# Kernel optimization log

Hardware: AMD Instinct MI355X
Metric: run time of the kernel (lower is better)

Reference implementation:

```python
import jax, jax.numpy as jnp
import numpy as np

# Static DAG: input -> L hidden layers of K nodes (dense between layers) -> output.
B, WIDTH, K, L = 262144, 64, 4, 4


def _linear_init(key, shape, fan_in):
    # matches nn.Linear default: U(-1/sqrt(fan_in), 1/sqrt(fan_in))
    bound = 1.0 / np.sqrt(fan_in)
    return jax.random.uniform(key, shape, jnp.float32, -bound, bound)


def setup_inputs() -> dict:
    key = jax.random.key(0)
    ks = jax.random.split(key, 9)
    x = jax.random.normal(ks[0], (B, WIDTH), jnp.float32)
    # input node -> first hidden layer (K edges)
    W_in = _linear_init(ks[1], (K, WIDTH, WIDTH), WIDTH)
    b_in = _linear_init(ks[2], (K, WIDTH), WIDTH)
    # between hidden layers: (L-1) transitions, K*K edges each; [pred, node, out, in]
    W_mid = _linear_init(ks[3], (L - 1, K, K, WIDTH, WIDTH), WIDTH)
    b_mid = _linear_init(ks[4], (L - 1, K, K, WIDTH), WIDTH)
    # last hidden layer -> output node (K edges)
    W_out = _linear_init(ks[5], (K, WIDTH, WIDTH), WIDTH)
    b_out = _linear_init(ks[6], (K, WIDTH), WIDTH)
    return {"x": x, "W_in": W_in, "b_in": b_in, "W_mid": W_mid,
            "b_mid": b_mid, "W_out": W_out, "b_out": b_out}


def _l2_normalize(t):
    # torch.linalg.norm(t) with no dim: Frobenius norm over the WHOLE tensor
    return t / jnp.linalg.norm(t)


def reference(x, W_in, b_in, W_mid, b_mid, W_out, b_out):
    # input node -> layer 1: each node k gets a single edge Linear, then normalize
    h = jnp.einsum('bw,kvw->kbv', x, W_in) + b_in[:, None, :]  # [K,B,W]
    h = jax.vmap(_l2_normalize)(h)
    # hidden -> hidden transitions: node v sums over its K predecessor edges
    for l in range(L - 1):  # small fixed structural loop over layers
        pre = jnp.einsum('pbw,pkvw->kbv', h, W_mid[l]) + b_mid[l].sum(axis=0)[:, None, :]
        h = jax.vmap(_l2_normalize)(pre)
    # last layer -> output node: sum K edge outputs, normalize
    out = jnp.einsum('pbw,pvw->bv', h, W_out) + b_out.sum(axis=0)
    return _l2_normalize(out)
```

## Files before the change

kernel.cpp:

```cpp
#include <hip/hip_runtime.h>


#define BF 262144.0f
#define SLOT 4608

#define OFF_G   0
#define OFF_S   4096
#define OFF_P2  8192
#define OFF_C2  73728
#define OFF_P4  74752
#define OFF_C4  91136
#define OFF_MO  91392
#define OFF_CO  95488

typedef __attribute__((ext_vector_type(8))) short bf16x8;
typedef __attribute__((ext_vector_type(4))) float f32x4;

__device__ __forceinline__ unsigned short f2bf(float f) {
  unsigned u = __builtin_bit_cast(unsigned, f);
  u += 0x7FFF + ((u >> 16) & 1);
  return (unsigned short)(u >> 16);
}
__device__ __forceinline__ float bf2f(unsigned short h) {
  unsigned u = ((unsigned)h) << 16;
  return __builtin_bit_cast(float, u);
}

__device__ __forceinline__ bf16x8 cvt8(f32x4 a, f32x4 b, float s) {
  bf16x8 t;
#pragma unroll
  for (int j = 0; j < 4; j++) {
    t[j]     = (short)f2bf(a[j] * s);
    t[j + 4] = (short)f2bf(b[j] * s);
  }
  return t;
}

__device__ __forceinline__ void split8(f32x4 a, f32x4 b, float sc,
                                       bf16x8& hi, bf16x8& lo) {
#pragma unroll
  for (int j = 0; j < 4; j++) {
    float v = a[j] * sc;
    unsigned short h = f2bf(v);
    hi[j] = (short)h; lo[j] = (short)f2bf(v - bf2f(h));
    v = b[j] * sc;
    h = f2bf(v);
    hi[j + 4] = (short)h; lo[j + 4] = (short)f2bf(v - bf2f(h));
  }
}

__device__ __forceinline__ float qpart(const unsigned short* th,
                                       const unsigned short* tl,
                                       int it, int col, int quad,
                                       const float Greg[4][4]) {
  f32x4 dq[4];
#pragma unroll
  for (int ut = 0; ut < 4; ut++) dq[ut] = (f32x4){0.f, 0.f, 0.f, 0.f};
#pragma unroll
  for (int ks = 0; ks < 2; ks++) {
    const bf16x8 ah = *(const bf16x8*)&th[(it * 16 + col) * 72 + ks * 32 + quad * 8];
    const bf16x8 al = *(const bf16x8*)&tl[(it * 16 + col) * 72 + ks * 32 + quad * 8];
#pragma unroll
    for (int ut = 0; ut < 4; ut++) {
      const bf16x8 bh = *(const bf16x8*)&th[(ut * 16 + col) * 72 + ks * 32 + quad * 8];
      const bf16x8 bl = *(const bf16x8*)&tl[(ut * 16 + col) * 72 + ks * 32 + quad * 8];
      dq[ut] = __builtin_amdgcn_mfma_f32_16x16x32_bf16(ah, bh, dq[ut], 0, 0, 0);
      dq[ut] = __builtin_amdgcn_mfma_f32_16x16x32_bf16(ah, bl, dq[ut], 0, 0, 0);
      dq[ut] = __builtin_amdgcn_mfma_f32_16x16x32_bf16(al, bh, dq[ut], 0, 0, 0);
    }
  }
  float qp = 0.f;
#pragma unroll
  for (int ut = 0; ut < 4; ut++)
#pragma unroll
    for (int r = 0; r < 4; r++) qp += dq[ut][r] * Greg[ut][r];
  return qp;
}

__device__ __forceinline__ void blkred(float qp, float* red4, float* qvv,
                                       int idx, int tid, int lane, int it) {
#pragma unroll
  for (int off = 32; off; off >>= 1) qp += __shfl_down(qp, off, 64);
  if (lane == 0) red4[it] = qp;
  __syncthreads();
  if (tid == 0) qvv[idx] = 1.0f / sqrtf(red4[0] + red4[1] + red4[2] + red4[3]);
  __syncthreads();
}

__global__ __launch_bounds__(256) void kG(const float* __restrict__ x,
                                          float* __restrict__ Gpart) {
  __shared__ __align__(16) unsigned short xts[4][4][16][8];
  __shared__ float sred[256][4];
  const int tid = threadIdx.x;
  const int lane = tid & 63, mt = tid >> 6;
  const int col = lane & 15, q = lane >> 4;
  const int row0 = tid >> 4;
  const int cf0  = (tid & 15) * 4;

  f32x4 acc[4];
#pragma unroll
  for (int nt = 0; nt < 4; nt++) acc[nt] = (f32x4){0.f, 0.f, 0.f, 0.f};
  float s0 = 0.f, s1 = 0.f, s2 = 0.f, s3 = 0.f;

  const float* bx = x + (long)blockIdx.x * 32768;
  f32x4 r0 = *(const f32x4*)(bx + tid * 4);
  f32x4 r1 = *(const f32x4*)(bx + 1024 + tid * 4);

  for (int c = 0; c < 16; c++) {
    __syncthreads();
    s0 += r0[0] + r1[0]; s1 += r0[1] + r1[1];
    s2 += r0[2] + r1[2]; s3 += r0[3] + r1[3];
#pragma unroll
    for (int j = 0; j < 4; j++) {
      const int cf = cf0 + j;
      xts[cf >> 4][row0 >> 3][cf & 15][row0 & 7]        = f2bf(r0[j]);
      xts[cf >> 4][2 + (row0 >> 3)][cf & 15][row0 & 7]  = f2bf(r1[j]);
    }
    f32x4 r0n = r0, r1n = r1;
    if (c < 15) {
      r0n = *(const f32x4*)(bx + (c + 1) * 2048 + tid * 4);
      r1n = *(const f32x4*)(bx + (c + 1) * 2048 + 1024 + tid * 4);
    }
    __syncthreads();
    const bf16x8 af = *(const bf16x8*)xts[mt][q][col];
#pragma unroll
    for (int nt = 0; nt < 4; nt++) {
      const bf16x8 bfr = *(const bf16x8*)xts[nt][q][col];
      acc[nt] = __builtin_amdgcn_mfma_f32_16x16x32_bf16(af, bfr, acc[nt], 0, 0, 0);
    }
    r0 = r0n; r1 = r1n;
  }

  float* myp = Gpart + (long)blockIdx.x * 4160;
#pragma unroll
  for (int nt = 0; nt < 4; nt++)
#pragma unroll
    for (int r = 0; r < 4; r++)
      myp[(mt * 16 + q * 4 + r) * 64 + nt * 16 + col] = acc[nt][r];

  sred[tid][0] = s0; sred[tid][1] = s1; sred[tid][2] = s2; sred[tid][3] = s3;
  __syncthreads();
  if (tid < 64) {
    float t = 0.f;
#pragma unroll
    for (int k2 = 0; k2 < 16; k2++) t += sred[(tid >> 2) + 16 * k2][tid & 3];
    myp[4096 + tid] = t;
  }
}

__global__ __launch_bounds__(256) void kGred(const float* __restrict__ Gpart,
                                             float* __restrict__ G,
                                             float* __restrict__ s) {
  __shared__ float red[4][64];
  const int tid = threadIdx.x;
  const int e = blockIdx.x * 64 + (tid & 63);
  const int quarter = tid >> 6;
  float acc = 0.f;
#pragma unroll 4
  for (int j = 0; j < 128; j++)
    acc += Gpart[(long)(quarter * 128 + j) * 4160 + e];
  red[quarter][tid & 63] = acc;
  __syncthreads();
  if (tid < 64) {
    const float t = red[0][tid] + red[1][tid] + red[2][tid] + red[3][tid];
    const int ee = blockIdx.x * 64 + tid;
    if (ee < 4096) G[ee] = t;
    else           s[ee - 4096] = t;
  }
}

__global__ __launch_bounds__(256) void kChainA(
    const float* __restrict__ Win, const float* __restrict__ bin,
    const float* __restrict__ Wm0, const float* __restrict__ bm0,
    const float* __restrict__ Wm1, const float* __restrict__ bm1,
    const float* __restrict__ G, const float* __restrict__ s,
    float* __restrict__ Pout, float* __restrict__ cpout) {
  extern __shared__ __align__(16) char smem[];
  unsigned short* Tth = (unsigned short*)smem;
  unsigned short* Ttl = Tth + 4 * SLOT;
  float* cAv  = (float*)(Ttl + 4 * SLOT);
  float* cBv  = cAv + 256;
  float* slv  = cBv + 64;
  float* red4 = slv + 64;
  float* qvv  = red4 + 4;

  const int tid = threadIdx.x;
  const int p2 = blockIdx.x >> 2, k2 = blockIdx.x & 3;
  const int lane = tid & 63, it = tid >> 6;
  const int col = lane & 15, quad = lane >> 4;

  float Greg[4][4];
#pragma unroll
  for (int ut = 0; ut < 4; ut++)
#pragma unroll
    for (int r = 0; r < 4; r++)
      Greg[ut][r] = G[(it * 16 + quad * 4 + r) * 64 + ut * 16 + col];
  if (tid < 64) slv[tid] = s[tid];
  if (tid < 256) cAv[tid] = bin[tid];

  {
    const int tc = tid >> 2, rb = (tid & 3) * 16;
#pragma unroll
    for (int p = 0; p < 4; p++)
#pragma unroll
      for (int j = 0; j < 16; j++) {
        const float tv = Win[p * 4096 + (rb + j) * 64 + tc];
        const unsigned short h = f2bf(tv);
        Tth[p * SLOT + tc * 72 + rb + j] = h;
        Ttl[p * SLOT + tc * 72 + rb + j] = f2bf(tv - bf2f(h));
      }
  }
  __syncthreads();

#pragma unroll
  for (int p = 0; p < 4; p++) {
    float qp = qpart(Tth + p * SLOT, Ttl + p * SLOT, it, col, quad, Greg);
    if (tid < 64) {
      float sd = 0.f;
      for (int w = 0; w < 64; w++)
        sd += slv[w] * (bf2f(Tth[p * SLOT + w * 72 + tid]) +
                        bf2f(Ttl[p * SLOT + w * 72 + tid]));
      const float c = cAv[p * 64 + tid];
      qp += c * (2.f * sd + BF * c);
    }
    blkred(qp, red4, qvv, p, tid, lane, it);
  }

  f32x4 dc[4];
#pragma unroll
  for (int nt = 0; nt < 4; nt++) dc[nt] = (f32x4){0.f, 0.f, 0.f, 0.f};
  float c2acc = 0.f;

  const int arow = it * 16 + col;
  f32x4 wr[4];
  {
    const float* wbase = Wm0 + (long)((0 * 4 + p2) * 64 + arow) * 64;
    wr[0] = *(const f32x4*)(wbase + quad * 8);
    wr[1] = *(const f32x4*)(wbase + quad * 8 + 4);
    wr[2] = *(const f32x4*)(wbase + 32 + quad * 8);
    wr[3] = *(const f32x4*)(wbase + 36 + quad * 8);
  }
#pragma unroll
  for (int p = 0; p < 4; p++) {
    const float inv = qvv[p];
    bf16x8 awh0, awl0, awh1, awl1;
    split8(wr[0], wr[1], inv, awh0, awl0);
    split8(wr[2], wr[3], inv, awh1, awl1);
    if (p < 3) {
      const float* wbase = Wm0 + (long)(((p + 1) * 4 + p2) * 64 + arow) * 64;
      wr[0] = *(const f32x4*)(wbase + quad * 8);
      wr[1] = *(const f32x4*)(wbase + quad * 8 + 4);
      wr[2] = *(const f32x4*)(wbase + 32 + quad * 8);
      wr[3] = *(const f32x4*)(wbase + 36 + quad * 8);
    }
#pragma unroll
    for (int nt = 0; nt < 4; nt++) {
      const bf16x8 bh0 = *(const bf16x8*)&Tth[p * SLOT + (nt * 16 + col) * 72 + quad * 8];
      const bf16x8 bl0 = *(const bf16x8*)&Ttl[p * SLOT + (nt * 16 + col) * 72 + quad * 8];
      dc[nt] = __builtin_amdgcn_mfma_f32_16x16x32_bf16(awh0, bh0, dc[nt], 0, 0, 0);
      dc[nt] = __builtin_amdgcn_mfma_f32_16x16x32_bf16(awh0, bl0, dc[nt], 0, 0, 0);
      dc[nt] = __builtin_amdgcn_mfma_f32_16x16x32_bf16(awl0, bh0, dc[nt], 0, 0, 0);
      const bf16x8 bh1 = *(const bf16x8*)&Tth[p * SLOT + (nt * 16 + col) * 72 + 32 + quad * 8];
      const bf16x8 bl1 = *(const bf16x8*)&Ttl[p * SLOT + (nt * 16 + col) * 72 + 32 + quad * 8];
      dc[nt] = __builtin_amdgcn_mfma_f32_16x16x32_bf16(awh1, bh1, dc[nt], 0, 0, 0);
      dc[nt] = __builtin_amdgcn_mfma_f32_16x16x32_bf16(awh1, bl1, dc[nt], 0, 0, 0);
      dc[nt] = __builtin_amdgcn_mfma_f32_16x16x32_bf16(awl1, bh1, dc[nt], 0, 0, 0);
    }
    if (tid < 64) {
      const float* wrow = Wm0 + (long)((p * 4 + p2) * 64 + tid) * 64;
      float pc = 0.f;
#pragma unroll
      for (int u4 = 0; u4 < 16; u4++) {
        const f32x4 wv = *(const f32x4*)(wrow + u4 * 4);
        pc += wv[0] * cAv[p * 64 + u4 * 4]     + wv[1] * cAv[p * 64 + u4 * 4 + 1] +
              wv[2] * cAv[p * 64 + u4 * 4 + 2] + wv[3] * cAv[p * 64 + u4 * 4 + 3];
      }
      c2acc += inv * pc + bm0[(p * 4 + p2) * 64 + tid];
    }
  }
  __syncthreads();

#pragma unroll
  for (int nt = 0; nt < 4; nt++)
#pragma unroll
    for (int r = 0; r < 4; r++) {
      const float val = dc[nt][r];
      const unsigned short h = f2bf(val);
      const int w_ = nt * 16 + col, v_ = it * 16 + quad * 4 + r;
      Tth[w_ * 72 + v_] = h;
      Ttl[w_ * 72 + v_] = f2bf(val - bf2f(h));
    }
  if (tid < 64) cBv[tid] = c2acc;
  __syncthreads();

  {
    float qp = qpart(Tth, Ttl, it, col, quad, Greg);
    if (tid < 64) {
      float sd = 0.f;
      for (int w = 0; w < 64; w++)
        sd += slv[w] * (bf2f(Tth[w * 72 + tid]) + bf2f(Ttl[w * 72 + tid]));
      const float c = cBv[tid];
      qp += c * (2.f * sd + BF * c);
    }
    blkred(qp, red4, qvv, 4, tid, lane, it);
  }
  const float inv2 = qvv[4];

  {
    f32x4 dcO[4];
#pragma unroll
    for (int nt = 0; nt < 4; nt++) dcO[nt] = (f32x4){0.f, 0.f, 0.f, 0.f};
    const float* wbase = Wm1 + (long)((p2 * 4 + k2) * 64 + arow) * 64;
    const f32x4 w0 = *(const f32x4*)(wbase + quad * 8);
    const f32x4 w1 = *(const f32x4*)(wbase + quad * 8 + 4);
    const f32x4 w2 = *(const f32x4*)(wbase + 32 + quad * 8);
    const f32x4 w3 = *(const f32x4*)(wbase + 36 + quad * 8);
    bf16x8 awh0, awl0, awh1, awl1;
    split8(w0, w1, inv2, awh0, awl0);
    split8(w2, w3, inv2, awh1, awl1);
#pragma unroll
    for (int nt = 0; nt < 4; nt++) {
      const bf16x8 bh0 = *(const bf16x8*)&Tth[(nt * 16 + col) * 72 + quad * 8];
      const bf16x8 bl0 = *(const bf16x8*)&Ttl[(nt * 16 + col) * 72 + quad * 8];
      dcO[nt] = __builtin_amdgcn_mfma_f32_16x16x32_bf16(awh0, bh0, dcO[nt], 0, 0, 0);
      dcO[nt] = __builtin_amdgcn_mfma_f32_16x16x32_bf16(awh0, bl0, dcO[nt], 0, 0, 0);
      dcO[nt] = __builtin_amdgcn_mfma_f32_16x16x32_bf16(awl0, bh0, dcO[nt], 0, 0, 0);
      const bf16x8 bh1 = *(const bf16x8*)&Tth[(nt * 16 + col) * 72 + 32 + quad * 8];
      const bf16x8 bl1 = *(const bf16x8*)&Ttl[(nt * 16 + col) * 72 + 32 + quad * 8];
      dcO[nt] = __builtin_amdgcn_mfma_f32_16x16x32_bf16(awh1, bh1, dcO[nt], 0, 0, 0);
      dcO[nt] = __builtin_amdgcn_mfma_f32_16x16x32_bf16(awh1, bl1, dcO[nt], 0, 0, 0);
      dcO[nt] = __builtin_amdgcn_mfma_f32_16x16x32_bf16(awl1, bh1, dcO[nt], 0, 0, 0);
    }
    float* po = Pout + (long)(p2 * 4 + k2) * 4096;
#pragma unroll
    for (int nt = 0; nt < 4; nt++)
#pragma unroll
      for (int r = 0; r < 4; r++)
        po[(it * 16 + quad * 4 + r) * 64 + nt * 16 + col] = dcO[nt][r];
    if (tid < 64) {
      const float* wrow = Wm1 + (long)((p2 * 4 + k2) * 64 + tid) * 64;
      float pc = 0.f;
#pragma unroll
      for (int u4 = 0; u4 < 16; u4++) {
        const f32x4 wv = *(const f32x4*)(wrow + u4 * 4);
        pc += wv[0] * cBv[u4 * 4]     + wv[1] * cBv[u4 * 4 + 1] +
              wv[2] * cBv[u4 * 4 + 2] + wv[3] * cBv[u4 * 4 + 3];
      }
      cpout[(p2 * 4 + k2) * 64 + tid] = inv2 * pc + bm1[(p2 * 4 + k2) * 64 + tid];
    }
  }
}

__global__ __launch_bounds__(256) void kChainB(
    const float* __restrict__ Pin, const float* __restrict__ cpin,
    const float* __restrict__ Wm2, const float* __restrict__ bm2,
    const float* __restrict__ Wout, const float* __restrict__ bout,
    const float* __restrict__ G, const float* __restrict__ s,
    float* __restrict__ Pout, float* __restrict__ cpout) {
  extern __shared__ __align__(16) char smem[];
  unsigned short* Tth = (unsigned short*)smem;
  unsigned short* Ttl = Tth + 4 * SLOT;
  float* cAv  = (float*)(Ttl + 4 * SLOT);
  float* cBv  = cAv + 256;
  float* slv  = cBv + 64;
  float* red4 = slv + 64;
  float* qvv  = red4 + 4;

  const int tid = threadIdx.x;
  const int kp = blockIdx.x;
  const int lane = tid & 63, it = tid >> 6;
  const int col = lane & 15, quad = lane >> 4;

  float Greg[4][4];
#pragma unroll
  for (int ut = 0; ut < 4; ut++)
#pragma unroll
    for (int r = 0; r < 4; r++)
      Greg[ut][r] = G[(it * 16 + quad * 4 + r) * 64 + ut * 16 + col];
  if (tid < 64) slv[tid] = s[tid];
  if (tid < 256) {
    const int k = tid >> 6, v = tid & 63;
    cAv[tid] = cpin[(0 * 4 + k) * 64 + v] + cpin[(1 * 4 + k) * 64 + v] +
               cpin[(2 * 4 + k) * 64 + v] + cpin[(3 * 4 + k) * 64 + v];
  }

  {
    const int tc = tid >> 2, rb = (tid & 3) * 16;
#pragma unroll
    for (int k = 0; k < 4; k++)
#pragma unroll
      for (int j = 0; j < 16; j++) {
        const int off = (rb + j) * 64 + tc;
        const float tv = Pin[(0 * 4 + k) * 4096 + off] + Pin[(1 * 4 + k) * 4096 + off] +
                         Pin[(2 * 4 + k) * 4096 + off] + Pin[(3 * 4 + k) * 4096 + off];
        const unsigned short h = f2bf(tv);
        Tth[k * SLOT + tc * 72 + rb + j] = h;
        Ttl[k * SLOT + tc * 72 + rb + j] = f2bf(tv - bf2f(h));
      }
  }
  __syncthreads();

#pragma unroll
  for (int k = 0; k < 4; k++) {
    float qp = qpart(Tth + k * SLOT, Ttl + k * SLOT, it, col, quad, Greg);
    if (tid < 64) {
      float sd = 0.f;
      for (int w = 0; w < 64; w++)
        sd += slv[w] * (bf2f(Tth[k * SLOT + w * 72 + tid]) +
                        bf2f(Ttl[k * SLOT + w * 72 + tid]));
      const float c = cAv[k * 64 + tid];
      qp += c * (2.f * sd + BF * c);
    }
    blkred(qp, red4, qvv, k, tid, lane, it);
  }

  f32x4 dc[4];
#pragma unroll
  for (int nt = 0; nt < 4; nt++) dc[nt] = (f32x4){0.f, 0.f, 0.f, 0.f};
  float c4acc = 0.f;

  const int arow = it * 16 + col;
  f32x4 wr[4];
  {
    const float* wbase = Wm2 + (long)((0 * 4 + kp) * 64 + arow) * 64;
    wr[0] = *(const f32x4*)(wbase + quad * 8);
    wr[1] = *(const f32x4*)(wbase + quad * 8 + 4);
    wr[2] = *(const f32x4*)(wbase + 32 + quad * 8);
    wr[3] = *(const f32x4*)(wbase + 36 + quad * 8);
  }
#pragma unroll
  for (int k = 0; k < 4; k++) {
    const float inv = qvv[k];
    bf16x8 awh0, awl0, awh1, awl1;
    split8(wr[0], wr[1], inv, awh0, awl0);
    split8(wr[2], wr[3], inv, awh1, awl1);
    if (k < 3) {
      const float* wbase = Wm2 + (long)(((k + 1) * 4 + kp) * 64 + arow) * 64;
      wr[0] = *(const f32x4*)(wbase + quad * 8);
      wr[1] = *(const f32x4*)(wbase + quad * 8 + 4);
      wr[2] = *(const f32x4*)(wbase + 32 + quad * 8);
      wr[3] = *(const f32x4*)(wbase + 36 + quad * 8);
    }
#pragma unroll
    for (int nt = 0; nt < 4; nt++) {
      const bf16x8 bh0 = *(const bf16x8*)&Tth[k * SLOT + (nt * 16 + col) * 72 + quad * 8];
      const bf16x8 bl0 = *(const bf16x8*)&Ttl[k * SLOT + (nt * 16 + col) * 72 + quad * 8];
      dc[nt] = __builtin_amdgcn_mfma_f32_16x16x32_bf16(awh0, bh0, dc[nt], 0, 0, 0);
      dc[nt] = __builtin_amdgcn_mfma_f32_16x16x32_bf16(awh0, bl0, dc[nt], 0, 0, 0);
      dc[nt] = __builtin_amdgcn_mfma_f32_16x16x32_bf16(awl0, bh0, dc[nt], 0, 0, 0);
      const bf16x8 bh1 = *(const bf16x8*)&Tth[k * SLOT + (nt * 16 + col) * 72 + 32 + quad * 8];
      const bf16x8 bl1 = *(const bf16x8*)&Ttl[k * SLOT + (nt * 16 + col) * 72 + 32 + quad * 8];
      dc[nt] = __builtin_amdgcn_mfma_f32_16x16x32_bf16(awh1, bh1, dc[nt], 0, 0, 0);
      dc[nt] = __builtin_amdgcn_mfma_f32_16x16x32_bf16(awh1, bl1, dc[nt], 0, 0, 0);
      dc[nt] = __builtin_amdgcn_mfma_f32_16x16x32_bf16(awl1, bh1, dc[nt], 0, 0, 0);
    }
    if (tid < 64) {
      const float* wrow = Wm2 + (long)((k * 4 + kp) * 64 + tid) * 64;
      float pc = 0.f;
#pragma unroll
      for (int u4 = 0; u4 < 16; u4++) {
        const f32x4 wv = *(const f32x4*)(wrow + u4 * 4);
        pc += wv[0] * cAv[k * 64 + u4 * 4]     + wv[1] * cAv[k * 64 + u4 * 4 + 1] +
              wv[2] * cAv[k * 64 + u4 * 4 + 2] + wv[3] * cAv[k * 64 + u4 * 4 + 3];
      }
      c4acc += inv * pc + bm2[(k * 4 + kp) * 64 + tid];
    }
  }
  __syncthreads();

#pragma unroll
  for (int nt = 0; nt < 4; nt++)
#pragma unroll
    for (int r = 0; r < 4; r++) {
      const float val = dc[nt][r];
      const unsigned short h = f2bf(val);
      const int w_ = nt * 16 + col, v_ = it * 16 + quad * 4 + r;
      Tth[w_ * 72 + v_] = h;
      Ttl[w_ * 72 + v_] = f2bf(val - bf2f(h));
    }
  if (tid < 64) cBv[tid] = c4acc;
  __syncthreads();

  {
    float qp = qpart(Tth, Ttl, it, col, quad, Greg);
    if (tid < 64) {
      float sd = 0.f;
      for (int w = 0; w < 64; w++)
        sd += slv[w] * (bf2f(Tth[w * 72 + tid]) + bf2f(Ttl[w * 72 + tid]));
      const float c = cBv[tid];
      qp += c * (2.f * sd + BF * c);
    }
    blkred(qp, red4, qvv, 4, tid, lane, it);
  }
  const float inv4 = qvv[4];

  {
    f32x4 dcO[4];
#pragma unroll
    for (int nt = 0; nt < 4; nt++) dcO[nt] = (f32x4){0.f, 0.f, 0.f, 0.f};
    const float* wbase = Wout + (long)(kp * 64 + arow) * 64;
    const f32x4 w0 = *(const f32x4*)(wbase + quad * 8);
    const f32x4 w1 = *(const f32x4*)(wbase + quad * 8 + 4);
    const f32x4 w2 = *(const f32x4*)(wbase + 32 + quad * 8);
    const f32x4 w3 = *(const f32x4*)(wbase + 36 + quad * 8);
    bf16x8 awh0, awl0, awh1, awl1;
    split8(w0, w1, inv4, awh0, awl0);
    split8(w2, w3, inv4, awh1, awl1);
#pragma unroll
    for (int nt = 0; nt < 4; nt++) {
      const bf16x8 bh0 = *(const bf16x8*)&Tth[(nt * 16 + col) * 72 + quad * 8];
      const bf16x8 bl0 = *(const bf16x8*)&Ttl[(nt * 16 + col) * 72 + quad * 8];
      dcO[nt] = __builtin_amdgcn_mfma_f32_16x16x32_bf16(awh0, bh0, dcO[nt], 0, 0, 0);
      dcO[nt] = __builtin_amdgcn_mfma_f32_16x16x32_bf16(awh0, bl0, dcO[nt], 0, 0, 0);
      dcO[nt] = __builtin_amdgcn_mfma_f32_16x16x32_bf16(awl0, bh0, dcO[nt], 0, 0, 0);
      const bf16x8 bh1 = *(const bf16x8*)&Tth[(nt * 16 + col) * 72 + 32 + quad * 8];
      const bf16x8 bl1 = *(const bf16x8*)&Ttl[(nt * 16 + col) * 72 + 32 + quad * 8];
      dcO[nt] = __builtin_amdgcn_mfma_f32_16x16x32_bf16(awh1, bh1, dcO[nt], 0, 0, 0);
      dcO[nt] = __builtin_amdgcn_mfma_f32_16x16x32_bf16(awh1, bl1, dcO[nt], 0, 0, 0);
      dcO[nt] = __builtin_amdgcn_mfma_f32_16x16x32_bf16(awl1, bh1, dcO[nt], 0, 0, 0);
    }
    float* po = Pout + (long)kp * 4096;
#pragma unroll
    for (int nt = 0; nt < 4; nt++)
#pragma unroll
      for (int r = 0; r < 4; r++)
        po[(it * 16 + quad * 4 + r) * 64 + nt * 16 + col] = dcO[nt][r];
    if (tid < 64) {
      const float* wrow = Wout + (long)(kp * 64 + tid) * 64;
      float pc = 0.f;
#pragma unroll
      for (int u4 = 0; u4 < 16; u4++) {
        const f32x4 wv = *(const f32x4*)(wrow + u4 * 4);
        pc += wv[0] * cBv[u4 * 4]     + wv[1] * cBv[u4 * 4 + 1] +
              wv[2] * cBv[u4 * 4 + 2] + wv[3] * cBv[u4 * 4 + 3];
      }
      cpout[kp * 64 + tid] = inv4 * pc + bout[kp * 64 + tid];
    }
  }
}

__global__ __launch_bounds__(256) void kNorm(const float* __restrict__ Psrc,
                                             const float* __restrict__ csrc,
                                             const float* __restrict__ G,
                                             const float* __restrict__ s,
                                             float* __restrict__ MoS,
                                             float* __restrict__ coS) {
  __shared__ float Tf[64][68];
  __shared__ __align__(16) unsigned short Tth[64][68], Ttl[64][68];
  __shared__ float red[256];
  __shared__ __align__(16) float cl[64], sl[64];
  const int tid = threadIdx.x;
  const int lane = tid & 63, it = tid >> 6;
  const int col = lane & 15, quad = lane >> 4;

  float Greg[4][4];
#pragma unroll
  for (int ut = 0; ut < 4; ut++)
#pragma unroll
    for (int r = 0; r < 4; r++)
      Greg[ut][r] = G[(it * 16 + quad * 4 + r) * 64 + ut * 16 + col];

#pragma unroll
  for (int m = 0; m < 16; m++) {
    const int li = m * 256 + tid;
    Tf[li >> 6][li & 63] = Psrc[li] + Psrc[4096 + li] + Psrc[8192 + li] + Psrc[12288 + li];
  }
  if (tid < 64) {
    cl[tid] = csrc[tid] + csrc[64 + tid] + csrc[128 + tid] + csrc[192 + tid];
    sl[tid] = s[tid];
  }
  __syncthreads();

  {
    const int tc = tid >> 2;
    const int rb = (tid & 3) * 16;
#pragma unroll
    for (int j = 0; j < 16; j++) {
      const float tv = Tf[rb + j][tc];
      const unsigned short h = f2bf(tv);
      Tth[tc][rb + j] = h;
      Ttl[tc][rb + j] = f2bf(tv - bf2f(h));
    }
  }
  __syncthreads();

  float qp = 0.f;
  {
    f32x4 dq[4];
#pragma unroll
    for (int ut = 0; ut < 4; ut++) dq[ut] = (f32x4){0.f, 0.f, 0.f, 0.f};
#pragma unroll
    for (int ks = 0; ks < 2; ks++) {
      const bf16x8 ah = *(const bf16x8*)&Tth[it * 16 + col][ks * 32 + quad * 8];
      const bf16x8 al = *(const bf16x8*)&Ttl[it * 16 + col][ks * 32 + quad * 8];
#pragma unroll
      for (int ut = 0; ut < 4; ut++) {
        const bf16x8 bh = *(const bf16x8*)&Tth[ut * 16 + col][ks * 32 + quad * 8];
        const bf16x8 bl = *(const bf16x8*)&Ttl[ut * 16 + col][ks * 32 + quad * 8];
        dq[ut] = __builtin_amdgcn_mfma_f32_16x16x32_bf16(ah, bh, dq[ut], 0, 0, 0);
        dq[ut] = __builtin_amdgcn_mfma_f32_16x16x32_bf16(ah, bl, dq[ut], 0, 0, 0);
        dq[ut] = __builtin_amdgcn_mfma_f32_16x16x32_bf16(al, bh, dq[ut], 0, 0, 0);
      }
    }
#pragma unroll
    for (int ut = 0; ut < 4; ut++)
#pragma unroll
      for (int r = 0; r < 4; r++)
        qp += dq[ut][r] * Greg[ut][r];
  }
  if (tid < 64) {
    float sd = 0.f;
#pragma unroll
    for (int u4 = 0; u4 < 16; u4++) {
      const f32x4 tv = *(const f32x4*)&Tf[tid][u4 * 4];
      const f32x4 sv = *(const f32x4*)&sl[u4 * 4];
      sd += sv[0] * tv[0] + sv[1] * tv[1] + sv[2] * tv[2] + sv[3] * tv[3];
    }
    qp += cl[tid] * (2.f * sd + BF * cl[tid]);
  }
  red[tid] = qp;
  __syncthreads();
  for (int st = 128; st > 0; st >>= 1) {
    if (tid < st) red[tid] += red[tid + st];
    __syncthreads();
  }
  const float inv = 1.0f / sqrtf(red[0]);

#pragma unroll
  for (int m = 0; m < 16; m++) {
    const int li = m * 256 + tid;
    MoS[li] = inv * Tf[li >> 6][li & 63];
  }
  if (tid < 64) coS[tid] = inv * cl[tid];
}

__global__ __launch_bounds__(256) void kApply(const float* __restrict__ x,
                                              const float* __restrict__ MoS,
                                              const float* __restrict__ coS,
                                              float* __restrict__ out) {
  const int tid = threadIdx.x, lane = tid & 63, vt = tid >> 6;
  const int col = lane & 15, q = lane >> 4;

  bf16x8 bfr[2];
  const float* mr = MoS + (vt * 16 + col) * 64 + q * 8;
  bfr[0] = cvt8(*(const f32x4*)mr, *(const f32x4*)(mr + 4), 1.f);
  bfr[1] = cvt8(*(const f32x4*)(mr + 32), *(const f32x4*)(mr + 36), 1.f);
  const float cf = coS[vt * 16 + col];

  for (int t = 0; t < 16; t++) {
    const int b0 = (blockIdx.x * 16 + t) * 16;
    const float* xr = x + (long)(b0 + col) * 64 + q * 8;
    const bf16x8 a0 = cvt8(*(const f32x4*)xr, *(const f32x4*)(xr + 4), 1.f);
    const bf16x8 a1 = cvt8(*(const f32x4*)(xr + 32), *(const f32x4*)(xr + 36), 1.f);
    f32x4 acc = (f32x4){0.f, 0.f, 0.f, 0.f};
    acc = __builtin_amdgcn_mfma_f32_16x16x32_bf16(a0, bfr[0], acc, 0, 0, 0);
    acc = __builtin_amdgcn_mfma_f32_16x16x32_bf16(a1, bfr[1], acc, 0, 0, 0);
#pragma unroll
    for (int r = 0; r < 4; r++)
      out[(long)(b0 + q * 4 + r) * 64 + vt * 16 + col] = acc[r] + cf;
  }
}

extern "C" void kernel_launch(void* const* d_in, const int* in_sizes, int n_in,
                              void* d_out, int out_size, void* d_ws, size_t ws_size,
                              hipStream_t stream) {
  const float* x    = (const float*)d_in[0];
  const float* Win  = (const float*)d_in[1];
  const float* bin  = (const float*)d_in[2];
  const float* Wmid = (const float*)d_in[3];
  const float* bmid = (const float*)d_in[4];
  const float* Wout = (const float*)d_in[5];
  const float* bout = (const float*)d_in[6];
  float* out = (float*)d_out;
  float* ws  = (float*)d_ws;
  float* Gpart = out;

  const size_t SMEM = (size_t)(8 * SLOT) * 2 + 396 * 4 + 64;
  hipFuncSetAttribute((const void*)kChainA,
                      hipFuncAttributeMaxDynamicSharedMemorySize, (int)SMEM);
  hipFuncSetAttribute((const void*)kChainB,
                      hipFuncAttributeMaxDynamicSharedMemorySize, (int)SMEM);

  kG   <<<512, 256, 0, stream>>>(x, Gpart);
  kGred<<<65, 256, 0, stream>>>(Gpart, ws + OFF_G, ws + OFF_S);
  kChainA<<<16, 256, SMEM, stream>>>(Win, bin, Wmid, bmid, Wmid + 65536, bmid + 1024,
                                     ws + OFF_G, ws + OFF_S, ws + OFF_P2, ws + OFF_C2);
  kChainB<<<4, 256, SMEM, stream>>>(ws + OFF_P2, ws + OFF_C2,
                                    Wmid + 131072, bmid + 2048, Wout, bout,
                                    ws + OFF_G, ws + OFF_S, ws + OFF_P4, ws + OFF_C4);
  kNorm<<<1, 256, 0, stream>>>(ws + OFF_P4, ws + OFF_C4, ws + OFF_G, ws + OFF_S,
                               ws + OFF_MO, ws + OFF_CO);
  kApply<<<1024, 256, 0, stream>>>(x, ws + OFF_MO, ws + OFF_CO, out);
}
```

Before: 230.8 us.

## Fuse final norm into last chain block and cache bf16 x for apply

The separate single-block normalization kernel is folded into kChainB: each block signals completion through an atomic counter, and the last block to finish computes the output norm and writes the scaled map. kG also writes a bf16 copy of x to workspace while converting it, so kApply reads half-width input instead of reloading fp32 x and converting it again. This removes one launch and halves kApply's input traffic. In exchange it adds a memset, an extra 32 MB of writes in kG, and a threadfence/atomic handshake.

```diff
diff --git a/kernel.cpp b/kernel.cpp
--- a/kernel.cpp
+++ b/kernel.cpp
@@ -12,9 +12,12 @@
 #define OFF_C4  91136
 #define OFF_MO  91392
 #define OFF_CO  95488
+#define OFF_CTR 95552
+#define OFF_X16 98304
 
 typedef __attribute__((ext_vector_type(8))) short bf16x8;
 typedef __attribute__((ext_vector_type(4))) float f32x4;
+typedef __attribute__((ext_vector_type(4))) unsigned short u16x4;
 
 __device__ __forceinline__ unsigned short f2bf(float f) {
   unsigned u = __builtin_bit_cast(unsigned, f);
@@ -88,7 +91,8 @@
 }
 
 __global__ __launch_bounds__(256) void kG(const float* __restrict__ x,
-                                          float* __restrict__ Gpart) {
+                                          float* __restrict__ Gpart,
+                                          unsigned short* __restrict__ x16) {
   __shared__ __align__(16) unsigned short xts[4][4][16][8];
   __shared__ float sred[256][4];
   const int tid = threadIdx.x;
@@ -102,7 +106,8 @@
   for (int nt = 0; nt < 4; nt++) acc[nt] = (f32x4){0.f, 0.f, 0.f, 0.f};
   float s0 = 0.f, s1 = 0.f, s2 = 0.f, s3 = 0.f;
 
-  const float* bx = x + (long)blockIdx.x * 32768;
+  const long brow = (long)blockIdx.x * 512;
+  const float* bx = x + brow * 64;
   f32x4 r0 = *(const f32x4*)(bx + tid * 4);
   f32x4 r1 = *(const f32x4*)(bx + 1024 + tid * 4);
 
@@ -110,12 +115,18 @@
     __syncthreads();
     s0 += r0[0] + r1[0]; s1 += r0[1] + r1[1];
     s2 += r0[2] + r1[2]; s3 += r0[3] + r1[3];
+    u16x4 h0, h1;
 #pragma unroll
     for (int j = 0; j < 4; j++) {
       const int cf = cf0 + j;
-      xts[cf >> 4][row0 >> 3][cf & 15][row0 & 7]        = f2bf(r0[j]);
-      xts[cf >> 4][2 + (row0 >> 3)][cf & 15][row0 & 7]  = f2bf(r1[j]);
-    }
+      const unsigned short b0 = f2bf(r0[j]);
+      const unsigned short b1 = f2bf(r1[j]);
+      h0[j] = b0; h1[j] = b1;
+      xts[cf >> 4][row0 >> 3][cf & 15][row0 & 7]        = b0;
+      xts[cf >> 4][2 + (row0 >> 3)][cf & 15][row0 & 7]  = b1;
+    }
+    *(u16x4*)(x16 + (brow + c * 32 + row0) * 64 + cf0)      = h0;
+    *(u16x4*)(x16 + (brow + c * 32 + 16 + row0) * 64 + cf0) = h1;
     f32x4 r0n = r0, r1n = r1;
     if (c < 15) {
       r0n = *(const f32x4*)(bx + (c + 1) * 2048 + tid * 4);
@@ -356,7 +367,9 @@
     const float* __restrict__ Wm2, const float* __restrict__ bm2,
     const float* __restrict__ Wout, const float* __restrict__ bout,
     const float* __restrict__ G, const float* __restrict__ s,
-    float* __restrict__ Pout, float* __restrict__ cpout) {
+    float* __restrict__ Pout, float* __restrict__ cpout,
+    float* __restrict__ MoS, float* __restrict__ coS,
+    int* __restrict__ ctr) {
   extern __shared__ __align__(16) char smem[];
   unsigned short* Tth = (unsigned short*)smem;
   unsigned short* Ttl = Tth + 4 * SLOT;
@@ -365,6 +378,7 @@
   float* slv  = cBv + 64;
   float* red4 = slv + 64;
   float* qvv  = red4 + 4;
+  __shared__ int isLast;
 
   const int tid = threadIdx.x;
   const int kp = blockIdx.x;
@@ -537,104 +551,56 @@
       cpout[kp * 64 + tid] = inv4 * pc + bout[kp * 64 + tid];
     }
   }
-}
-
-__global__ __launch_bounds__(256) void kNorm(const float* __restrict__ Psrc,
-                                             const float* __restrict__ csrc,
-                                             const float* __restrict__ G,
-                                             const float* __restrict__ s,
-                                             float* __restrict__ MoS,
-                                             float* __restrict__ coS) {
-  __shared__ float Tf[64][68];
-  __shared__ __align__(16) unsigned short Tth[64][68], Ttl[64][68];
-  __shared__ float red[256];
-  __shared__ __align__(16) float cl[64], sl[64];
-  const int tid = threadIdx.x;
-  const int lane = tid & 63, it = tid >> 6;
-  const int col = lane & 15, quad = lane >> 4;
-
-  float Greg[4][4];
-#pragma unroll
-  for (int ut = 0; ut < 4; ut++)
-#pragma unroll
-    for (int r = 0; r < 4; r++)
-      Greg[ut][r] = G[(it * 16 + quad * 4 + r) * 64 + ut * 16 + col];
-
+
+  __threadfence();
+  __syncthreads();
+  if (tid == 0) isLast = (atomicAdd(ctr, 1) == 3);
+  __syncthreads();
+  if (!isLast) return;
+  __threadfence();
+
+  float* Tfin = (float*)(Tth + 2 * SLOT);
 #pragma unroll
   for (int m = 0; m < 16; m++) {
     const int li = m * 256 + tid;
-    Tf[li >> 6][li & 63] = Psrc[li] + Psrc[4096 + li] + Psrc[8192 + li] + Psrc[12288 + li];
-  }
-  if (tid < 64) {
-    cl[tid] = csrc[tid] + csrc[64 + tid] + csrc[128 + tid] + csrc[192 + tid];
-    sl[tid] = s[tid];
-  }
-  __syncthreads();
-
-  {
-    const int tc = tid >> 2;
-    const int rb = (tid & 3) * 16;
+    Tfin[(li >> 6) * 68 + (li & 63)] =
+        Pout[li] + Pout[4096 + li] + Pout[8192 + li] + Pout[12288 + li];
+  }
+  if (tid < 64)
+    cBv[tid] = cpout[tid] + cpout[64 + tid] + cpout[128 + tid] + cpout[192 + tid];
+  __syncthreads();
+  {
+    const int tc = tid >> 2, rb = (tid & 3) * 16;
 #pragma unroll
     for (int j = 0; j < 16; j++) {
-      const float tv = Tf[rb + j][tc];
+      const float tv = Tfin[(rb + j) * 68 + tc];
       const unsigned short h = f2bf(tv);
-      Tth[tc][rb + j] = h;
-      Ttl[tc][rb + j] = f2bf(tv - bf2f(h));
-    }
-  }
-  __syncthreads();
-
-  float qp = 0.f;
-  {
-    f32x4 dq[4];
-#pragma unroll
-    for (int ut = 0; ut < 4; ut++) dq[ut] = (f32x4){0.f, 0.f, 0.f, 0.f};
-#pragma unroll
-    for (int ks = 0; ks < 2; ks++) {
-      const bf16x8 ah = *(const bf16x8*)&Tth[it * 16 + col][ks * 32 + quad * 8];
-      const bf16x8 al = *(const bf16x8*)&Ttl[it * 16 + col][ks * 32 + quad * 8];
-#pragma unroll
-      for (int ut = 0; ut < 4; ut++) {
-        const bf16x8 bh = *(const bf16x8*)&Tth[ut * 16 + col][ks * 32 + quad * 8];
-        const bf16x8 bl = *(const bf16x8*)&Ttl[ut * 16 + col][ks * 32 + quad * 8];
-        dq[ut] = __builtin_amdgcn_mfma_f32_16x16x32_bf16(ah, bh, dq[ut], 0, 0, 0);
-        dq[ut] = __builtin_amdgcn_mfma_f32_16x16x32_bf16(ah, bl, dq[ut], 0, 0, 0);
-        dq[ut] = __builtin_amdgcn_mfma_f32_16x16x32_bf16(al, bh, dq[ut], 0, 0, 0);
-      }
-    }
-#pragma unroll
-    for (int ut = 0; ut < 4; ut++)
-#pragma unroll
-      for (int r = 0; r < 4; r++)
-        qp += dq[ut][r] * Greg[ut][r];
-  }
-  if (tid < 64) {
-    float sd = 0.f;
-#pragma unroll
-    for (int u4 = 0; u4 < 16; u4++) {
-      const f32x4 tv = *(const f32x4*)&Tf[tid][u4 * 4];
-      const f32x4 sv = *(const f32x4*)&sl[u4 * 4];
-      sd += sv[0] * tv[0] + sv[1] * tv[1] + sv[2] * tv[2] + sv[3] * tv[3];
-    }
-    qp += cl[tid] * (2.f * sd + BF * cl[tid]);
-  }
-  red[tid] = qp;
-  __syncthreads();
-  for (int st = 128; st > 0; st >>= 1) {
-    if (tid < st) red[tid] += red[tid + st];
-    __syncthreads();
-  }
-  const float inv = 1.0f / sqrtf(red[0]);
-
+      Tth[tc * 72 + rb + j] = h;
+      Ttl[tc * 72 + rb + j] = f2bf(tv - bf2f(h));
+    }
+  }
+  __syncthreads();
+  {
+    float qp = qpart(Tth, Ttl, it, col, quad, Greg);
+    if (tid < 64) {
+      float sd = 0.f;
+      for (int w = 0; w < 64; w++)
+        sd += slv[w] * (bf2f(Tth[w * 72 + tid]) + bf2f(Ttl[w * 72 + tid]));
+      const float c = cBv[tid];
+      qp += c * (2.f * sd + BF * c);
+    }
+    blkred(qp, red4, qvv, 5, tid, lane, it);
+  }
+  const float invo = qvv[5];
 #pragma unroll
   for (int m = 0; m < 16; m++) {
     const int li = m * 256 + tid;
-    MoS[li] = inv * Tf[li >> 6][li & 63];
-  }
-  if (tid < 64) coS[tid] = inv * cl[tid];
-}
-
-__global__ __launch_bounds__(256) void kApply(const float* __restrict__ x,
+    MoS[li] = invo * Tfin[(li >> 6) * 68 + (li & 63)];
+  }
+  if (tid < 64) coS[tid] = invo * cBv[tid];
+}
+
+__global__ __launch_bounds__(256) void kApply(const unsigned short* __restrict__ x16,
                                               const float* __restrict__ MoS,
                                               const float* __restrict__ coS,
                                               float* __restrict__ out) {
@@ -649,9 +615,9 @@
 
   for (int t = 0; t < 16; t++) {
     const int b0 = (blockIdx.x * 16 + t) * 16;
-    const float* xr = x + (long)(b0 + col) * 64 + q * 8;
-    const bf16x8 a0 = cvt8(*(const f32x4*)xr, *(const f32x4*)(xr + 4), 1.f);
-    const bf16x8 a1 = cvt8(*(const f32x4*)(xr + 32), *(const f32x4*)(xr + 36), 1.f);
+    const unsigned short* xr = x16 + (long)(b0 + col) * 64 + q * 8;
+    const bf16x8 a0 = *(const bf16x8*)xr;
+    const bf16x8 a1 = *(const bf16x8*)(xr + 32);
     f32x4 acc = (f32x4){0.f, 0.f, 0.f, 0.f};
     acc = __builtin_amdgcn_mfma_f32_16x16x32_bf16(a0, bfr[0], acc, 0, 0, 0);
     acc = __builtin_amdgcn_mfma_f32_16x16x32_bf16(a1, bfr[1], acc, 0, 0, 0);
@@ -674,6 +640,8 @@
   float* out = (float*)d_out;
   float* ws  = (float*)d_ws;
   float* Gpart = out;
+  unsigned short* x16 = (unsigned short*)(ws + OFF_X16);
+  int* ctr = (int*)(ws + OFF_CTR);
 
   const size_t SMEM = (size_t)(8 * SLOT) * 2 + 396 * 4 + 64;
   hipFuncSetAttribute((const void*)kChainA,
@@ -681,14 +649,14 @@
   hipFuncSetAttribute((const void*)kChainB,
                       hipFuncAttributeMaxDynamicSharedMemorySize, (int)SMEM);
 
-  kG   <<<512, 256, 0, stream>>>(x, Gpart);
+  hipMemsetAsync(ctr, 0, sizeof(int), stream);
+  kG   <<<512, 256, 0, stream>>>(x, Gpart, x16);
   kGred<<<65, 256, 0, stream>>>(Gpart, ws + OFF_G, ws + OFF_S);
   kChainA<<<16, 256, SMEM, stream>>>(Win, bin, Wmid, bmid, Wmid + 65536, bmid + 1024,
                                      ws + OFF_G, ws + OFF_S, ws + OFF_P2, ws + OFF_C2);
   kChainB<<<4, 256, SMEM, stream>>>(ws + OFF_P2, ws + OFF_C2,
                                     Wmid + 131072, bmid + 2048, Wout, bout,
-                                    ws + OFF_G, ws + OFF_S, ws + OFF_P4, ws + OFF_C4);
-  kNorm<<<1, 256, 0, stream>>>(ws + OFF_P4, ws + OFF_C4, ws + OFF_G, ws + OFF_S,
-                               ws + OFF_MO, ws + OFF_CO);
-  kApply<<<1024, 256, 0, stream>>>(x, ws + OFF_MO, ws + OFF_CO, out);
-}
+                                    ws + OFF_G, ws + OFF_S, ws + OFF_P4, ws + OFF_C4,
+                                    ws + OFF_MO, ws + OFF_CO, ctr);
+  kApply<<<1024, 256, 0, stream>>>(x16, ws + OFF_MO, ws + OFF_CO, out);
+}
```

New measurement: 240.6 us. 4.3% more time.
